# Kernel tuning notes

Hardware: AMD Instinct MI355X
Metric: run time of the kernel (lower is better)

## Reference

```python
import jax, jax.numpy as jnp
import numpy as np

N = 50000   # nodes
E = 800000  # edges (avg degree 16)
C = 128     # in_channels
B = 8       # graphs in batch


def setup_inputs() -> dict:
    key = jax.random.key(0)
    k1, k2, k3, k4, k5 = jax.random.split(key, 5)
    x = jax.random.normal(k1, (N, C), dtype=jnp.float32)
    src = jax.random.randint(k2, (E,), 0, N)
    off = jax.random.randint(k3, (E,), 1, N)
    dst = (src + off) % N  # guarantees no self-loops -> self-loop filter is identity
    edge_index = jnp.stack([src, dst]).astype(jnp.int32)
    batch = jnp.sort(jax.random.randint(k4, (N,), 0, B)).astype(jnp.int32)
    # torch.nn.Linear(2C, 1): weight [1, 2C] stored flat as w[2C], bias b[1]
    w = jax.random.normal(k5, (2 * C,), dtype=jnp.float32) * (1.0 / np.sqrt(2 * C))
    b = jnp.zeros((1,), dtype=jnp.float32)
    return {"x": x, "edge_index": edge_index, "batch": batch, "w": w, "b": b}


def _connected_components(src, dst, emask, num_nodes):
    """Weakly-connected components via min-label propagation + pointer jumping.
    Returns labels in [0, num_nodes): the min node index of each component."""
    labels = jnp.arange(num_nodes, dtype=jnp.int32)
    iters = int(np.ceil(np.log2(max(num_nodes, 2)))) + 4
    big = jnp.int32(num_nodes)

    def body(_, lab):
        m = jnp.minimum(lab[src], lab[dst])
        upd = jnp.where(emask, m, big)
        lab = lab.at[src].min(upd)
        lab = lab.at[dst].min(upd)
        return lab[lab]  # pointer jump

    return jax.lax.fori_loop(0, iters, body, labels)


def reference(x, edge_index, batch, w, b):
    n, c = x.shape
    src, dst = edge_index[0], edge_index[1]
    # lin(cat(x[src], x[dst])) == x[src]@w[:c] + x[dst]@w[c:] + b (avoids E x 2c concat)
    edge_score = jnp.tanh(x[src] @ w[:c] + x[dst] @ w[c:] + b[0])  # [E]
    contract = edge_score > 0.0  # threshold for tanh is 0.0
    cluster = _connected_components(src, dst, contract, n)  # [n], label = min node idx
    # nodes untouched by any contracted edge keep their own feature (S[i,i]=1)
    ci = contract.astype(jnp.int32)
    deg = jnp.zeros((n,), jnp.int32).at[src].add(ci).at[dst].add(ci)
    single = deg == 0
    # sx = S @ x done sparsely: each edge (u,v,s) adds s * x[v] to row u
    sx = jnp.zeros_like(x).at[src].add(edge_score[:, None] * x[dst])
    sx = sx + jnp.where(single[:, None], x, jnp.zeros_like(x))
    # x_out = C^T (S @ x): sum rows within each cluster (padded to n rows for static shape)
    x_out = jax.ops.segment_sum(sx, cluster, num_segments=n)  # [n, c]
    # coarse edges: clusters of original endpoints (un-deduplicated; diag entries are
    # the ones dense_to_sparse(fill_diagonal_(0)) would drop)
    edge_index_out = jnp.stack([cluster[src], cluster[dst]])  # [2, E]
    batch_out = jnp.zeros((n,), batch.dtype).at[cluster].set(batch)  # padded to n
    return x_out, edge_index_out, batch_out, cluster
```

## Files before the change

### kernel.cpp

```cpp
#include <hip/hip_runtime.h>

constexpr int Cc = 128;
constexpr int NB = 1024;
constexpr int CH = 128;
constexpr int MAXIT = 6;

__global__ void k_node_dots(const float* __restrict__ x, const float* __restrict__ w,
                            const float* __restrict__ bptr, float* __restrict__ xw1,
                            float* __restrict__ xw2, int N) {
  int wid = (blockIdx.x * blockDim.x + threadIdx.x) >> 6;
  int lane = threadIdx.x & 63;
  if (wid >= N) return;
  const float2* xr = (const float2*)(x + (size_t)wid * Cc);
  const float2* w2 = (const float2*)w;
  float2 v = xr[lane];
  float2 wa = w2[lane];
  float2 wb = w2[lane + 64];
  float s1 = v.x * wa.x + v.y * wa.y;
  float s2 = v.x * wb.x + v.y * wb.y;
#pragma unroll
  for (int off = 32; off >= 1; off >>= 1) {
    s1 += __shfl_xor(s1, off);
    s2 += __shfl_xor(s2, off);
  }
  if (lane == 0) {
    xw1[wid] = s1 + bptr[0];
    xw2[wid] = s2;
  }
}

__global__ void k_score_hist(const int* __restrict__ src, const int* __restrict__ dst,
                             const float* __restrict__ xw1, const float* __restrict__ xw2,
                             float* __restrict__ score, int* __restrict__ T1,
                             int* __restrict__ T2, int* __restrict__ lab, int E, int N) {
  __shared__ int h1[NB], h2[NB];
  for (int i = threadIdx.x; i < NB; i += blockDim.x) {
    h1[i] = 0;
    h2[i] = 0;
  }
  for (int v = blockIdx.x * blockDim.x + threadIdx.x; v < N; v += gridDim.x * blockDim.x)
    lab[v] = v;
  __syncthreads();
  int ch = (E + gridDim.x - 1) / gridDim.x;
  int lo = blockIdx.x * ch, hi = min(lo + ch, E);
  for (int e = lo + threadIdx.x; e < hi; e += blockDim.x) {
    int s = src[e];
    int d = dst[e];
    float arg = xw1[s] + xw2[d];
    score[e] = tanhf(arg);
    atomicAdd(&h1[s >> 6], 1);
    if (arg > 0.0f) {
      atomicAdd(&h2[s >> 6], 1);
      atomicAdd(&h2[d >> 6], 1);
    }
  }
  __syncthreads();
  for (int i = threadIdx.x; i < NB; i += blockDim.x) {
    T1[blockIdx.x * NB + i] = h1[i];
    T2[blockIdx.x * NB + i] = h2[i];
  }
}

__global__ void k_colsum(const int* __restrict__ T1, const int* __restrict__ T2,
                         int* __restrict__ cs, int C) {
  int wid = (blockIdx.x * blockDim.x + threadIdx.x) >> 6;
  int lane = threadIdx.x & 63;
  if (wid >= 2 * NB) return;
  const int* T = (wid < NB) ? T1 : T2;
  int b = wid & (NB - 1);
  int s = 0;
  for (int c = lane; c < C; c += 64) s += T[c * NB + b];
#pragma unroll
  for (int off = 32; off >= 1; off >>= 1) s += __shfl_xor(s, off);
  if (lane == 0) cs[wid] = s;
}

__global__ void k_scanB(const int* __restrict__ cs, int* __restrict__ bb1,
                        int* __restrict__ bb2) {
  __shared__ int part[1024];
  int t = threadIdx.x;
  int v = cs[t];
  part[t] = v;
  __syncthreads();
  for (int d = 1; d < 1024; d <<= 1) {
    int u = (t >= d) ? part[t - d] : 0;
    __syncthreads();
    part[t] += u;
    __syncthreads();
  }
  bb1[t] = part[t] - v;
  if (t == 1023) bb1[1024] = part[t];
  __syncthreads();
  v = cs[1024 + t];
  part[t] = v;
  __syncthreads();
  for (int d = 1; d < 1024; d <<= 1) {
    int u = (t >= d) ? part[t - d] : 0;
    __syncthreads();
    part[t] += u;
    __syncthreads();
  }
  bb2[t] = part[t] - v;
  if (t == 1023) bb2[1024] = part[t];
}

__global__ void k_chunkscan(int* __restrict__ T1, const int* __restrict__ bb1,
                            int* __restrict__ T2, const int* __restrict__ bb2, int C) {
  int wid = (blockIdx.x * blockDim.x + threadIdx.x) >> 6;
  int lane = threadIdx.x & 63;
  if (wid >= 2 * NB) return;
  int* T = (wid < NB) ? T1 : T2;
  const int* bb = (wid < NB) ? bb1 : bb2;
  int b = wid & (NB - 1);
  int c0 = 2 * lane, c1 = 2 * lane + 1;
  int a0 = (c0 < C) ? T[c0 * NB + b] : 0;
  int a1 = (c1 < C) ? T[c1 * NB + b] : 0;
  int loc = a0 + a1;
  int inc = loc;
#pragma unroll
  for (int off = 1; off < 64; off <<= 1) {
    int u = __shfl_up(inc, off);
    if (lane >= off) inc += u;
  }
  int excl = inc - loc;
  int base = bb[b];
  if (c0 < C) T[c0 * NB + b] = base + excl;
  if (c1 < C) T[c1 * NB + b] = base + excl + a0;
}

__global__ void k_scat2(const int* __restrict__ src, const int* __restrict__ dst,
                        const float* __restrict__ score, const int* __restrict__ T1,
                        const int* __restrict__ T2, int* __restrict__ pk,
                        int2* __restrict__ pay, int2* __restrict__ apair, int E) {
  __shared__ int cur1[NB], cur2[NB];
  for (int i = threadIdx.x; i < NB; i += blockDim.x) {
    cur1[i] = T1[blockIdx.x * NB + i];
    cur2[i] = T2[blockIdx.x * NB + i];
  }
  __syncthreads();
  int ch = (E + gridDim.x - 1) / gridDim.x;
  int lo = blockIdx.x * ch, hi = min(lo + ch, E);
  for (int e = lo + threadIdx.x; e < hi; e += blockDim.x) {
    int s = src[e];
    int d = dst[e];
    float t = score[e];
    int slot = atomicAdd(&cur1[s >> 6], 1);
    pk[slot] = s;
    pay[slot] = make_int2(d, __float_as_int(t));
    if (t > 0.0f) {
      int s2 = atomicAdd(&cur2[s >> 6], 1);
      apair[s2] = make_int2(s, d);
      int s3 = atomicAdd(&cur2[d >> 6], 1);
      apair[s3] = make_int2(d, s);
    }
  }
}

__global__ void k_bucket2(const int* __restrict__ pk, const int2* __restrict__ pay,
                          const int* __restrict__ bb1, int* __restrict__ cnt_src,
                          int* __restrict__ csr_off, int2* __restrict__ pack,
                          const int2* __restrict__ apair, const int* __restrict__ bb2,
                          int* __restrict__ adj_off, int* __restrict__ adj_cnt,
                          int* __restrict__ adj, int nb, int N) {
  __shared__ int h[64], off_s[64], cur[64];
  int b = blockIdx.x;
  if (b < nb) {
    int lo = bb1[b], hi = bb1[b + 1];
    if (threadIdx.x < 64) h[threadIdx.x] = 0;
    __syncthreads();
    for (int i = lo + threadIdx.x; i < hi; i += blockDim.x) atomicAdd(&h[pk[i] & 63], 1);
    __syncthreads();
    if (threadIdx.x == 0) {
      int run = lo;
      for (int j = 0; j < 64; ++j) {
        off_s[j] = run;
        run += h[j];
      }
    }
    __syncthreads();
    if (threadIdx.x < 64) {
      cur[threadIdx.x] = off_s[threadIdx.x];
      int g = (b << 6) + threadIdx.x;
      if (g < N) {
        csr_off[g] = off_s[threadIdx.x];
        cnt_src[g] = h[threadIdx.x];
      }
    }
    __syncthreads();
    for (int i = lo + threadIdx.x; i < hi; i += blockDim.x) {
      int2 p = pay[i];
      int slot = atomicAdd(&cur[pk[i] & 63], 1);
      pack[slot] = p;
    }
  } else {
    b -= nb;
    int lo = bb2[b], hi = bb2[b + 1];
    if (threadIdx.x < 64) h[threadIdx.x] = 0;
    __syncthreads();
    for (int i = lo + threadIdx.x; i < hi; i += blockDim.x)
      atomicAdd(&h[apair[i].x & 63], 1);
    __syncthreads();
    if (threadIdx.x == 0) {
      int run = lo;
      for (int j = 0; j < 64; ++j) {
        off_s[j] = run;
        run += h[j];
      }
    }
    __syncthreads();
    if (threadIdx.x < 64) {
      cur[threadIdx.x] = off_s[threadIdx.x];
      int g = (b << 6) + threadIdx.x;
      if (g < N) {
        adj_off[g] = off_s[threadIdx.x];
        adj_cnt[g] = h[threadIdx.x];
      }
    }
    __syncthreads();
    for (int i = lo + threadIdx.x; i < hi; i += blockDim.x) {
      int2 p = apair[i];
      int slot = atomicAdd(&cur[p.x & 63], 1);
      adj[slot] = p.y;
    }
  }
}

__global__ void k_cc_node(const int* __restrict__ adj_off, const int* __restrict__ adj_cnt,
                          const int* __restrict__ adj, int* __restrict__ lab,
                          int* __restrict__ flags, int it, int N) {
  if (it > 0 && flags[it - 1] == 0) return;
  int tid = blockIdx.x * blockDim.x + threadIdx.x;
  int stride = gridDim.x * blockDim.x;
  bool ch = false;
#pragma unroll
  for (int s = 0; s < 2; ++s) {
    for (int v = tid; v < N; v += stride) {
      int a = lab[v];
      int b = lab[a];
      int c = lab[b];
      int m = min(a, min(b, c));
      int beg = adj_off[v], num = adj_cnt[v];
      for (int k = 0; k < num; ++k) m = min(m, lab[adj[beg + k]]);
      if (m < a) {
        lab[v] = m;
        ch = true;
      }
    }
  }
  if (ch) flags[it] = 1;
}

__global__ void k_sx_csr(const int2* __restrict__ pack, const int* __restrict__ csr_off,
                         const int* __restrict__ cnt_src, const int* __restrict__ adj_cnt,
                         const float* __restrict__ x, float* __restrict__ sx, int N) {
  int wid = (blockIdx.x * blockDim.x + threadIdx.x) >> 6;
  int lane = threadIdx.x & 63;
  if (wid >= N) return;
  int beg = csr_off[wid], num = cnt_src[wid];
  float ax = 0.f, ay = 0.f;
  int k = 0;
  if ((beg & 1) && num > 0) {
    int2 p = pack[beg];
    float t = __int_as_float(p.y);
    float2 v = ((const float2*)(x + (size_t)p.x * Cc))[lane];
    ax += t * v.x;
    ay += t * v.y;
    k = 1;
  }
  for (; k + 3 < num; k += 4) {
    int4 p0 = *((const int4*)(pack + beg + k));
    int4 p1 = *((const int4*)(pack + beg + k + 2));
    float t0 = __int_as_float(p0.y);
    float t1 = __int_as_float(p0.w);
    float t2 = __int_as_float(p1.y);
    float t3 = __int_as_float(p1.w);
    float2 v0 = ((const float2*)(x + (size_t)p0.x * Cc))[lane];
    float2 v1 = ((const float2*)(x + (size_t)p0.z * Cc))[lane];
    float2 v2 = ((const float2*)(x + (size_t)p1.x * Cc))[lane];
    float2 v3 = ((const float2*)(x + (size_t)p1.z * Cc))[lane];
    ax += t0 * v0.x + t1 * v1.x + t2 * v2.x + t3 * v3.x;
    ay += t0 * v0.y + t1 * v1.y + t2 * v2.y + t3 * v3.y;
  }
  for (; k + 1 < num; k += 2) {
    int4 pp = *((const int4*)(pack + beg + k));
    float t0 = __int_as_float(pp.y);
    float t1 = __int_as_float(pp.w);
    float2 v0 = ((const float2*)(x + (size_t)pp.x * Cc))[lane];
    float2 v1 = ((const float2*)(x + (size_t)pp.z * Cc))[lane];
    ax += t0 * v0.x + t1 * v1.x;
    ay += t0 * v0.y + t1 * v1.y;
  }
  if (k < num) {
    int2 p = pack[beg + k];
    float t = __int_as_float(p.y);
    float2 v = ((const float2*)(x + (size_t)p.x * Cc))[lane];
    ax += t * v.x;
    ay += t * v.y;
  }
  if (adj_cnt[wid] == 0) {
    float2 v = ((const float2*)(x + (size_t)wid * Cc))[lane];
    ax += v.x;
    ay += v.y;
  }
  ((float2*)(sx + (size_t)wid * Cc))[lane] = make_float2(ax, ay);
}

__global__ void k_finish(const float* __restrict__ sx, const int* __restrict__ lab,
                         float* __restrict__ xout, const int* __restrict__ src,
                         const int* __restrict__ dst, const int* __restrict__ batch,
                         float* __restrict__ out_ei, float* __restrict__ out_cluster,
                         float* __restrict__ out_batch, int E, int N, int segBlocks) {
  int lane = threadIdx.x & 63;
  if ((int)blockIdx.x < segBlocks) {
    const int CHUNK = 128;
    int wv = threadIdx.x >> 6;
    int u0 = (blockIdx.x * 4 + wv) * CHUNK;
    if (u0 >= N) return;
    int u1 = min(u0 + CHUNK, N);
    int prevc = lab[u0];
    float ax = 0.f, ay = 0.f;
    for (int u = u0; u < u1; ++u) {
      int c = lab[u];
      float2 v = ((const float2*)(sx + (size_t)u * Cc))[lane];
      if (c != prevc) {
        float* row = xout + (size_t)prevc * Cc + 2 * lane;
        atomicAdd(row, ax);
        atomicAdd(row + 1, ay);
        ax = 0.f;
        ay = 0.f;
        prevc = c;
      }
      ax += v.x;
      ay += v.y;
    }
    float* row = xout + (size_t)prevc * Cc + 2 * lane;
    atomicAdd(row, ax);
    atomicAdd(row + 1, ay);
    return;
  }
  int i = (blockIdx.x - segBlocks) * blockDim.x + threadIdx.x;
  if (i < E) {
    out_ei[i] = (float)lab[src[i]];
    out_ei[E + i] = (float)lab[dst[i]];
  }
  bool valid = i < N;
  int c = valid ? lab[i] : -1;
  float bv = valid ? (float)batch[i] : -1.f;
  if (valid) out_cluster[i] = (float)c;
  unsigned long long remaining = __ballot(valid);
  while (remaining) {
    int leader = __ffsll((unsigned long long)remaining) - 1;
    int lc = __shfl(c, leader);
    bool mine = valid && (c == lc);
    unsigned long long grp = __ballot(mine);
    float v = mine ? bv : -1.f;
#pragma unroll
    for (int off = 32; off >= 1; off >>= 1) v = fmaxf(v, __shfl_xor(v, off));
    if (lane == leader) atomicMax((int*)&out_batch[lc], __float_as_int(v));
    remaining &= ~grp;
  }
}

extern "C" void kernel_launch(void* const* d_in, const int* in_sizes, int n_in,
                              void* d_out, int out_size, void* d_ws, size_t ws_size,
                              hipStream_t stream) {
  const float* x = (const float*)d_in[0];
  const int* ei = (const int*)d_in[1];
  const int* batch = (const int*)d_in[2];
  const float* w = (const float*)d_in[3];
  const float* b = (const float*)d_in[4];
  const int N = in_sizes[2];
  const int E = in_sizes[1] / 2;
  const int* src = ei;
  const int* dst = ei + E;
  const int nb = (N + 63) >> 6;

  char* ws = (char*)d_ws;
  size_t off = 0;
  auto alloc = [&](size_t bytes) -> void* {
    void* p = ws + off;
    off = (off + bytes + 255) & ~(size_t)255;
    return p;
  };
  int* flags = (int*)alloc((size_t)MAXIT * 4);
  const size_t zero_bytes = off;
  float* xw1 = (float*)alloc((size_t)N * 4);
  float* xw2 = (float*)alloc((size_t)N * 4);
  float* score = (float*)alloc((size_t)E * 4);
  int* lab = (int*)alloc((size_t)N * 4);
  int* cnt_src = (int*)alloc((size_t)N * 4);
  int* csr_off = (int*)alloc((size_t)N * 4);
  int* adj_off = (int*)alloc((size_t)N * 4);
  int* adj_cnt = (int*)alloc((size_t)N * 4);
  int* T1 = (int*)alloc((size_t)CH * NB * 4);
  int* T2 = (int*)alloc((size_t)CH * NB * 4);
  int* bb1 = (int*)alloc((size_t)(NB + 1) * 4);
  int* bb2 = (int*)alloc((size_t)(NB + 1) * 4);
  int* cs = (int*)alloc((size_t)2 * NB * 4);
  int* pk = (int*)alloc((size_t)E * 4);
  int2* pack = (int2*)alloc((size_t)E * 8);
  float* sx = (float*)alloc((size_t)N * Cc * 4);
  int2* apair = (int2*)sx;
  int* adj = (int*)((char*)sx + (size_t)E * 16);
  int2* pay;
  if (32 * (size_t)E <= (size_t)N * Cc * 4) {
    pay = (int2*)((char*)sx + (size_t)E * 24);
  } else {
    pay = (int2*)alloc((size_t)E * 8);
  }
  (void)ws_size;

  float* out_x = (float*)d_out;
  float* out_ei = out_x + (size_t)N * Cc;
  float* out_batch = out_ei + 2 * (size_t)E;
  float* out_cluster = out_batch + N;

  hipMemsetAsync(d_out, 0, (size_t)out_size * 4, stream);
  hipMemsetAsync(d_ws, 0, zero_bytes, stream);

  k_node_dots<<<(N + 3) / 4, 256, 0, stream>>>(x, w, b, xw1, xw2, N);
  k_score_hist<<<CH, 256, 0, stream>>>(src, dst, xw1, xw2, score, T1, T2, lab, E, N);
  k_colsum<<<(2 * NB) / 4, 256, 0, stream>>>(T1, T2, cs, CH);
  k_scanB<<<1, 1024, 0, stream>>>(cs, bb1, bb2);
  k_chunkscan<<<(2 * NB) / 4, 256, 0, stream>>>(T1, bb1, T2, bb2, CH);
  k_scat2<<<CH, 256, 0, stream>>>(src, dst, score, T1, T2, pk, pay, apair, E);
  k_bucket2<<<2 * nb, 256, 0, stream>>>(pk, pay, bb1, cnt_src, csr_off, pack, apair, bb2,
                                        adj_off, adj_cnt, adj, nb, N);
  for (int it = 0; it < MAXIT; ++it) {
    k_cc_node<<<(N + 255) / 256, 256, 0, stream>>>(adj_off, adj_cnt, adj, lab, flags, it, N);
  }
  k_sx_csr<<<(N + 3) / 4, 256, 0, stream>>>(pack, csr_off, cnt_src, adj_cnt, x, sx, N);
  {
    int segBlocks = (N + 511) / 512;
    int outBlocks = (E + 255) / 256;
    k_finish<<<segBlocks + outBlocks, 256, 0, stream>>>(sx, lab, out_x, src, dst, batch,
                                                        out_ei, out_cluster, out_batch, E, N,
                                                        segBlocks);
  }
}
```

Before: 292.7 us.

## Fuse sx computation with cluster segment reduction via block partials

```diff
diff --git a/kernel.cpp b/kernel.cpp
--- a/kernel.cpp
+++ b/kernel.cpp
@@ -250,95 +250,126 @@
   if (ch) flags[it] = 1;
 }
 
-__global__ void k_sx_csr(const int2* __restrict__ pack, const int* __restrict__ csr_off,
-                         const int* __restrict__ cnt_src, const int* __restrict__ adj_cnt,
-                         const float* __restrict__ x, float* __restrict__ sx, int N) {
-  int wid = (blockIdx.x * blockDim.x + threadIdx.x) >> 6;
-  int lane = threadIdx.x & 63;
-  if (wid >= N) return;
-  int beg = csr_off[wid], num = cnt_src[wid];
+__global__ __launch_bounds__(1024) void k_sx_fused(
+    const int2* __restrict__ pack, const int* __restrict__ csr_off,
+    const int* __restrict__ cnt_src, const int* __restrict__ adj_cnt,
+    const int* __restrict__ lab, const float* __restrict__ x, float* __restrict__ xout,
+    float* __restrict__ part, int* __restrict__ plab, int N) {
+  __shared__ float sf[16][128];
+  __shared__ int slab[16];
+  int wv = threadIdx.x >> 6, lane = threadIdx.x & 63;
+  int wid = blockIdx.x * 16 + wv;
   float ax = 0.f, ay = 0.f;
-  int k = 0;
-  if ((beg & 1) && num > 0) {
-    int2 p = pack[beg];
-    float t = __int_as_float(p.y);
-    float2 v = ((const float2*)(x + (size_t)p.x * Cc))[lane];
-    ax += t * v.x;
-    ay += t * v.y;
-    k = 1;
-  }
-  for (; k + 3 < num; k += 4) {
-    int4 p0 = *((const int4*)(pack + beg + k));
-    int4 p1 = *((const int4*)(pack + beg + k + 2));
-    float t0 = __int_as_float(p0.y);
-    float t1 = __int_as_float(p0.w);
-    float t2 = __int_as_float(p1.y);
-    float t3 = __int_as_float(p1.w);
-    float2 v0 = ((const float2*)(x + (size_t)p0.x * Cc))[lane];
-    float2 v1 = ((const float2*)(x + (size_t)p0.z * Cc))[lane];
-    float2 v2 = ((const float2*)(x + (size_t)p1.x * Cc))[lane];
-    float2 v3 = ((const float2*)(x + (size_t)p1.z * Cc))[lane];
-    ax += t0 * v0.x + t1 * v1.x + t2 * v2.x + t3 * v3.x;
-    ay += t0 * v0.y + t1 * v1.y + t2 * v2.y + t3 * v3.y;
-  }
-  for (; k + 1 < num; k += 2) {
-    int4 pp = *((const int4*)(pack + beg + k));
-    float t0 = __int_as_float(pp.y);
-    float t1 = __int_as_float(pp.w);
-    float2 v0 = ((const float2*)(x + (size_t)pp.x * Cc))[lane];
-    float2 v1 = ((const float2*)(x + (size_t)pp.z * Cc))[lane];
-    ax += t0 * v0.x + t1 * v1.x;
-    ay += t0 * v0.y + t1 * v1.y;
-  }
-  if (k < num) {
-    int2 p = pack[beg + k];
-    float t = __int_as_float(p.y);
-    float2 v = ((const float2*)(x + (size_t)p.x * Cc))[lane];
-    ax += t * v.x;
-    ay += t * v.y;
-  }
-  if (adj_cnt[wid] == 0) {
-    float2 v = ((const float2*)(x + (size_t)wid * Cc))[lane];
-    ax += v.x;
-    ay += v.y;
-  }
-  ((float2*)(sx + (size_t)wid * Cc))[lane] = make_float2(ax, ay);
-}
-
-__global__ void k_finish(const float* __restrict__ sx, const int* __restrict__ lab,
-                         float* __restrict__ xout, const int* __restrict__ src,
-                         const int* __restrict__ dst, const int* __restrict__ batch,
-                         float* __restrict__ out_ei, float* __restrict__ out_cluster,
-                         float* __restrict__ out_batch, int E, int N, int segBlocks) {
-  int lane = threadIdx.x & 63;
-  if ((int)blockIdx.x < segBlocks) {
-    const int CHUNK = 128;
-    int wv = threadIdx.x >> 6;
-    int u0 = (blockIdx.x * 4 + wv) * CHUNK;
-    if (u0 >= N) return;
-    int u1 = min(u0 + CHUNK, N);
-    int prevc = lab[u0];
-    float ax = 0.f, ay = 0.f;
-    for (int u = u0; u < u1; ++u) {
-      int c = lab[u];
-      float2 v = ((const float2*)(sx + (size_t)u * Cc))[lane];
+  int labv = -1;
+  if (wid < N) {
+    labv = lab[wid];
+    int beg = csr_off[wid], num = cnt_src[wid];
+    int k = 0;
+    if ((beg & 1) && num > 0) {
+      int2 p = pack[beg];
+      float t = __int_as_float(p.y);
+      float2 v = ((const float2*)(x + (size_t)p.x * Cc))[lane];
+      ax += t * v.x;
+      ay += t * v.y;
+      k = 1;
+    }
+    for (; k + 3 < num; k += 4) {
+      int4 p0 = *((const int4*)(pack + beg + k));
+      int4 p1 = *((const int4*)(pack + beg + k + 2));
+      float t0 = __int_as_float(p0.y);
+      float t1 = __int_as_float(p0.w);
+      float t2 = __int_as_float(p1.y);
+      float t3 = __int_as_float(p1.w);
+      float2 v0 = ((const float2*)(x + (size_t)p0.x * Cc))[lane];
+      float2 v1 = ((const float2*)(x + (size_t)p0.z * Cc))[lane];
+      float2 v2 = ((const float2*)(x + (size_t)p1.x * Cc))[lane];
+      float2 v3 = ((const float2*)(x + (size_t)p1.z * Cc))[lane];
+      ax += t0 * v0.x + t1 * v1.x + t2 * v2.x + t3 * v3.x;
+      ay += t0 * v0.y + t1 * v1.y + t2 * v2.y + t3 * v3.y;
+    }
+    for (; k + 1 < num; k += 2) {
+      int4 pp = *((const int4*)(pack + beg + k));
+      float t0 = __int_as_float(pp.y);
+      float t1 = __int_as_float(pp.w);
+      float2 v0 = ((const float2*)(x + (size_t)pp.x * Cc))[lane];
+      float2 v1 = ((const float2*)(x + (size_t)pp.z * Cc))[lane];
+      ax += t0 * v0.x + t1 * v1.x;
+      ay += t0 * v0.y + t1 * v1.y;
+    }
+    if (k < num) {
+      int2 p = pack[beg + k];
+      float t = __int_as_float(p.y);
+      float2 v = ((const float2*)(x + (size_t)p.x * Cc))[lane];
+      ax += t * v.x;
+      ay += t * v.y;
+    }
+    if (adj_cnt[wid] == 0) {
+      float2 v = ((const float2*)(x + (size_t)wid * Cc))[lane];
+      ax += v.x;
+      ay += v.y;
+    }
+  }
+  sf[wv][2 * lane] = ax;
+  sf[wv][2 * lane + 1] = ay;
+  if (lane == 0) slab[wv] = labv;
+  __syncthreads();
+  if (threadIdx.x < 128) {
+    int j = threadIdx.x;
+    int prevc = slab[0];
+    float acc = 0.f;
+#pragma unroll
+    for (int r = 0; r < 16; ++r) {
+      int c = slab[r];
+      float v = sf[r][j];
       if (c != prevc) {
+        if (prevc >= 0) atomicAdd(&xout[(size_t)prevc * Cc + j], acc);
+        acc = 0.f;
+        prevc = c;
+      }
+      acc += v;
+    }
+    part[(size_t)blockIdx.x * Cc + j] = acc;
+    if (j == 0) plab[blockIdx.x] = prevc;
+  }
+}
+
+__global__ void k_reduce(const float* __restrict__ part, const int* __restrict__ plab,
+                         float* __restrict__ xout, int P) {
+  int wv = threadIdx.x >> 6, lane = threadIdx.x & 63;
+  int r0 = (blockIdx.x * 4 + wv) * 32;
+  if (r0 >= P) return;
+  int r1 = min(r0 + 32, P);
+  int prevc = plab[r0];
+  float ax = 0.f, ay = 0.f;
+  for (int r = r0; r < r1; ++r) {
+    int c = plab[r];
+    float2 v = ((const float2*)(part + (size_t)r * Cc))[lane];
+    if (c != prevc) {
+      if (prevc >= 0) {
         float* row = xout + (size_t)prevc * Cc + 2 * lane;
         atomicAdd(row, ax);
         atomicAdd(row + 1, ay);
-        ax = 0.f;
-        ay = 0.f;
-        prevc = c;
-      }
-      ax += v.x;
-      ay += v.y;
-    }
+      }
+      ax = 0.f;
+      ay = 0.f;
+      prevc = c;
+    }
+    ax += v.x;
+    ay += v.y;
+  }
+  if (prevc >= 0) {
     float* row = xout + (size_t)prevc * Cc + 2 * lane;
     atomicAdd(row, ax);
     atomicAdd(row + 1, ay);
-    return;
-  }
-  int i = (blockIdx.x - segBlocks) * blockDim.x + threadIdx.x;
+  }
+}
+
+__global__ void k_finish(const int* __restrict__ lab, const int* __restrict__ src,
+                         const int* __restrict__ dst, const int* __restrict__ batch,
+                         float* __restrict__ out_ei, float* __restrict__ out_cluster,
+                         float* __restrict__ out_batch, int E, int N) {
+  int i = blockIdx.x * blockDim.x + threadIdx.x;
+  int lane = threadIdx.x & 63;
   if (i < E) {
     out_ei[i] = (float)lab[src[i]];
     out_ei[E + i] = (float)lab[dst[i]];
@@ -374,6 +405,7 @@
   const int* src = ei;
   const int* dst = ei + E;
   const int nb = (N + 63) >> 6;
+  const int P = (N + 15) / 16;
 
   char* ws = (char*)d_ws;
   size_t off = 0;
@@ -399,15 +431,17 @@
   int* cs = (int*)alloc((size_t)2 * NB * 4);
   int* pk = (int*)alloc((size_t)E * 4);
   int2* pack = (int2*)alloc((size_t)E * 8);
-  float* sx = (float*)alloc((size_t)N * Cc * 4);
-  int2* apair = (int2*)sx;
-  int* adj = (int*)((char*)sx + (size_t)E * 16);
+  char* scr = (char*)alloc((size_t)N * Cc * 4);
+  int2* apair = (int2*)scr;
+  int* adj = (int*)(scr + (size_t)E * 16);
   int2* pay;
   if (32 * (size_t)E <= (size_t)N * Cc * 4) {
-    pay = (int2*)((char*)sx + (size_t)E * 24);
+    pay = (int2*)(scr + (size_t)E * 24);
   } else {
     pay = (int2*)alloc((size_t)E * 8);
   }
+  float* part = (float*)scr;
+  int* plab = (int*)(scr + (size_t)P * Cc * 4);
   (void)ws_size;
 
   float* out_x = (float*)d_out;
@@ -415,7 +449,8 @@
   float* out_batch = out_ei + 2 * (size_t)E;
   float* out_cluster = out_batch + N;
 
-  hipMemsetAsync(d_out, 0, (size_t)out_size * 4, stream);
+  hipMemsetAsync(out_x, 0, (size_t)N * Cc * 4, stream);
+  hipMemsetAsync(out_batch, 0, (size_t)N * 4, stream);
   hipMemsetAsync(d_ws, 0, zero_bytes, stream);
 
   k_node_dots<<<(N + 3) / 4, 256, 0, stream>>>(x, w, b, xw1, xw2, N);
@@ -429,12 +464,12 @@
   for (int it = 0; it < MAXIT; ++it) {
     k_cc_node<<<(N + 255) / 256, 256, 0, stream>>>(adj_off, adj_cnt, adj, lab, flags, it, N);
   }
-  k_sx_csr<<<(N + 3) / 4, 256, 0, stream>>>(pack, csr_off, cnt_src, adj_cnt, x, sx, N);
+  k_sx_fused<<<P, 1024, 0, stream>>>(pack, csr_off, cnt_src, adj_cnt, lab, x, out_x, part,
+                                     plab, N);
   {
-    int segBlocks = (N + 511) / 512;
-    int outBlocks = (E + 255) / 256;
-    k_finish<<<segBlocks + outBlocks, 256, 0, stream>>>(sx, lab, out_x, src, dst, batch,
-                                                        out_ei, out_cluster, out_batch, E, N,
-                                                        segBlocks);
-  }
-}
+    int waves = (P + 31) / 32;
+    k_reduce<<<(waves + 3) / 4, 256, 0, stream>>>(part, plab, out_x, P);
+  }
+  k_finish<<<(E + 255) / 256, 256, 0, stream>>>(lab, src, dst, batch, out_ei, out_cluster,
+                                                out_batch, E, N);
+}
```

Measured after the change: 270.3 us. 1.08x faster.
